# Performance work log

Measured on AMD Instinct MI355X. Metric: run time of the kernel, lower is better.

## Reference

```python
import jax, jax.numpy as jnp
import numpy as np

B = 4096
N_BUS = 118
N = B * N_BUS
E_ND = 4 * N
E = E_ND + N
REF_NODE = 0
NUM_GNN_LAYERS = 10


def setup_inputs() -> dict:
    key = jax.random.key(0)
    ks = jax.random.split(key, 8)
    x = jax.random.normal(ks[0], (N, 2), dtype=jnp.float32)
    y = jax.random.normal(ks[1], (N, 1), dtype=jnp.float32)
    edge_index_no_diag = jax.random.randint(ks[2], (2, E_ND), 0, N, dtype=jnp.int64)
    edge_attr_no_diag = jax.random.normal(ks[3], (E_ND,), dtype=jnp.float32)
    edge_index = jax.random.randint(ks[4], (2, E), 0, N, dtype=jnp.int64)
    edge_attr = jax.random.normal(ks[5], (E,), dtype=jnp.float32)
    ybus = jax.random.normal(ks[6], (B, N_BUS, N_BUS), dtype=jnp.float32)
    # ensure nonzero diagonal (bus self-admittance), as in real ybus matrices
    diag = 1.0 + jax.random.uniform(ks[7], (B, N_BUS), dtype=jnp.float32)
    ii = jnp.arange(N_BUS)
    ybus = ybus.at[:, ii, ii].set(diag)
    return {"x": x, "y": y, "edge_index_no_diag": edge_index_no_diag,
            "edge_attr_no_diag": edge_attr_no_diag, "edge_index": edge_index,
            "edge_attr": edge_attr, "ybus": ybus}


def _scatter_msg(theta, edge_index, edge_w):
    # message: y_j * edge_weight * 100, aggregated (add) at target node i
    src, dst = edge_index[0], edge_index[1]
    msg = theta[src, 0] * (edge_w * 100.0)
    return jax.ops.segment_sum(msg, dst, num_segments=N)[:, None]  # [N,1]


def reference(x, y, edge_index_no_diag, edge_attr_no_diag, edge_index, edge_attr, ybus):
    p = (x[:, 0] - x[:, 1])[:, None]                               # [N,1] net power injection
    denom = (jnp.diagonal(ybus, axis1=1, axis2=2) * 100.0).reshape(-1, 1)  # [N,1]

    def gpg_layer(theta):
        aggr = _scatter_msg(theta, edge_index_no_diag, edge_attr_no_diag)
        out = (p - aggr) / denom                                   # [N,1]
        o = out.reshape(B, N_BUS)
        o = o - o[:, REF_NODE:REF_NODE + 1]                        # subtract slack-bus angle
        return o.reshape(-1, 1)

    def lc_error(theta):
        aggr = _scatter_msg(theta, edge_index, edge_attr)
        return jnp.abs(p - aggr).sum()

    theta = jnp.zeros_like(y)
    out = gpg_layer(theta)
    errors = [lc_error(out)]
    for _ in range(NUM_GNN_LAYERS):
        out = gpg_layer(out)
        errors.append(lc_error(out))
    return out, jnp.stack(errors)
```

## Files before the change

kernel.cpp:

```cpp
#include <hip/hip_runtime.h>

#define NBUS 118
#define BATCH 4096
#define NN (BATCH * NBUS)
#define END_E (4 * NN)
#define EF_E (END_E + NN)
#define NLAYERS 10

#define NBKT 236
#define SPAN_SHIFT 11
#define SPAN_MASK 2047
#define TILE 4096
#define ND_TILES (END_E / TILE)
#define F_TILES  (EF_E / TILE)
#define CAP_ND 8960
#define CAP_F  11008

__global__ void init_kernel(const float* __restrict__ x,
                            const float* __restrict__ ybus,
                            float* __restrict__ p,
                            float* __restrict__ denomInv,
                            int* __restrict__ cursor_nd,
                            int* __restrict__ cursor_f,
                            float* __restrict__ errOut) {
    int tid = blockIdx.x * blockDim.x + threadIdx.x;
    int stride = gridDim.x * blockDim.x;
    for (int i = tid; i < NN; i += stride) {
        float2 xi = ((const float2*)x)[i];
        p[i] = xi.x - xi.y;
        int b = i / NBUS;
        int j = i - b * NBUS;
        denomInv[i] = 1.0f / (ybus[b * (NBUS * NBUS) + j * (NBUS + 1)] * 100.0f);
    }
    if (tid < 256) {
        cursor_nd[tid] = tid * CAP_ND;
        cursor_f[tid]  = tid * CAP_F;
    }
    if (tid < NLAYERS + 1) errOut[tid] = 0.0f;
}

__global__ __launch_bounds__(256) void binA_kernel(
        const int* __restrict__ src_nd, const int* __restrict__ dst_nd,
        const float* __restrict__ ea_nd,
        const int* __restrict__ src_f, const int* __restrict__ dst_f,
        const float* __restrict__ ea_f,
        int* __restrict__ cursor_nd, int* __restrict__ cursor_f,
        uint2* __restrict__ stg_nd, uint2* __restrict__ stg_f) {
    __shared__ uint2 buf[TILE];
    __shared__ unsigned char sb[TILE];
    __shared__ int hist[256];
    __shared__ int scanA[256];
    __shared__ int segStart[256];
    __shared__ int segGBase[256];

    bool isF = blockIdx.x >= ND_TILES;
    int tile = isF ? (blockIdx.x - ND_TILES) : blockIdx.x;
    const int* src = isF ? src_f : src_nd;
    const int* dst = isF ? dst_f : dst_nd;
    const float* ea = isF ? ea_f : ea_nd;
    int* cursor = isF ? cursor_f : cursor_nd;
    uint2* stg = isF ? stg_f : stg_nd;
    int cap = isF ? CAP_F : CAP_ND;

    int tid = threadIdx.x;
    int base = tile * TILE;

    hist[tid] = 0;
    __syncthreads();

    #pragma unroll
    for (int k = 0; k < TILE / 256; ++k) {
        int d = dst[base + k * 256 + tid];
        atomicAdd(&hist[d >> SPAN_SHIFT], 1);
    }
    __syncthreads();

    int cnt = hist[tid];
    scanA[tid] = cnt;
    __syncthreads();
    for (int off = 1; off < 256; off <<= 1) {
        int t = (tid >= off) ? scanA[tid - off] : 0;
        __syncthreads();
        scanA[tid] += t;
        __syncthreads();
    }
    int excl = scanA[tid] - cnt;
    segStart[tid] = excl;
    hist[tid] = excl;
    if (tid < NBKT && cnt > 0) segGBase[tid] = atomicAdd(&cursor[tid], cnt);
    __syncthreads();

    #pragma unroll
    for (int k = 0; k < TILE / 256; ++k) {
        int e = base + k * 256 + tid;
        int d = dst[e];
        int bkt = d >> SPAN_SHIFT;
        int pos = atomicAdd(&hist[bkt], 1);
        unsigned dl = (unsigned)(d & SPAN_MASK);
        buf[pos] = make_uint2((unsigned)src[e] | (dl << 19),
                              (unsigned)__float_as_int(ea[e] * 100.0f));
        sb[pos] = (unsigned char)bkt;
    }
    __syncthreads();

    #pragma unroll
    for (int k = 0; k < TILE / 256; ++k) {
        int slot = k * 256 + tid;
        int bkt = sb[slot];
        int gpos = segGBase[bkt] + (slot - segStart[bkt]);
        if (gpos < (bkt + 1) * cap)
            stg[gpos] = buf[slot];
    }
}

__global__ void bucket_base_kernel(const int* __restrict__ cursor_nd,
                                   const int* __restrict__ cursor_f,
                                   int* __restrict__ base_nd,
                                   int* __restrict__ base_f,
                                   int* __restrict__ start_nd,
                                   int* __restrict__ start_f) {
    __shared__ int sd[256];
    int tid = threadIdx.x;
    int c = 0;
    if (tid < NBKT) {
        c = cursor_nd[tid] - tid * CAP_ND;
        if (c > CAP_ND) c = CAP_ND;
    }
    sd[tid] = c;
    __syncthreads();
    for (int off = 1; off < 256; off <<= 1) {
        int t = (tid >= off) ? sd[tid - off] : 0;
        __syncthreads();
        sd[tid] += t;
        __syncthreads();
    }
    if (tid < NBKT) base_nd[tid] = sd[tid] - c;
    __syncthreads();
    if (tid < NBKT) {
        c = cursor_f[tid] - tid * CAP_F;
        if (c > CAP_F) c = CAP_F;
    } else c = 0;
    sd[tid] = c;
    __syncthreads();
    for (int off = 1; off < 256; off <<= 1) {
        int t = (tid >= off) ? sd[tid - off] : 0;
        __syncthreads();
        sd[tid] += t;
        __syncthreads();
    }
    if (tid < NBKT) base_f[tid] = sd[tid] - c;
    if (tid == 0) {
        start_nd[NN] = END_E;
        start_f[NN] = EF_E;
    }
}

__global__ __launch_bounds__(256) void binB_kernel(
        const uint2* __restrict__ stg_nd, const uint2* __restrict__ stg_f,
        const int* __restrict__ cursor_nd, const int* __restrict__ cursor_f,
        const int* __restrict__ base_nd, const int* __restrict__ base_f,
        int* __restrict__ start_nd, int* __restrict__ start_f,
        int2* __restrict__ perm_nd, int2* __restrict__ perm_f) {
    __shared__ int h[2048];
    __shared__ int partial[256];

    bool isF = blockIdx.x >= NBKT;
    int bb = isF ? (blockIdx.x - NBKT) : blockIdx.x;
    const uint2* stg = isF ? stg_f : stg_nd;
    int cap = isF ? CAP_F : CAP_ND;
    int cnt = (isF ? cursor_f[bb] : cursor_nd[bb]) - bb * cap;
    if (cnt > cap) cnt = cap;
    int denseBase = isF ? base_f[bb] : base_nd[bb];
    int* start = isF ? start_f : start_nd;
    int2* perm = isF ? perm_f : perm_nd;
    int stgBase = bb * cap;
    int tid = threadIdx.x;

    #pragma unroll
    for (int k = 0; k < 8; ++k) h[k * 256 + tid] = 0;
    __syncthreads();

    for (int i = tid; i < cnt; i += 256) {
        uint2 v = stg[stgBase + i];
        atomicAdd(&h[(v.x >> 19) & SPAN_MASK], 1);
    }
    __syncthreads();

    int loc[8];
    int s = 0;
    #pragma unroll
    for (int k = 0; k < 8; ++k) { loc[k] = h[tid * 8 + k]; s += loc[k]; }
    partial[tid] = s;
    __syncthreads();
    for (int off = 1; off < 256; off <<= 1) {
        int t = (tid >= off) ? partial[tid - off] : 0;
        __syncthreads();
        partial[tid] += t;
        __syncthreads();
    }
    int run = partial[tid] - s;
    #pragma unroll
    for (int k = 0; k < 8; ++k) { int c = loc[k]; h[tid * 8 + k] = run; run += c; }
    __syncthreads();

    int nodeBase = bb * 2048;
    #pragma unroll
    for (int k = 0; k < 8; ++k) {
        int l = k * 256 + tid;
        start[nodeBase + l] = denseBase + h[l];
    }
    __syncthreads();

    for (int i = tid; i < cnt; i += 256) {
        uint2 v = stg[stgBase + i];
        int dl = (v.x >> 19) & SPAN_MASK;
        int pos = denseBase + atomicAdd(&h[dl], 1);
        perm[pos] = make_int2((int)(v.x & 0x7FFFF), (int)v.y);
    }
}

__global__ void out0_kernel(const float* __restrict__ p,
                            const float* __restrict__ denomInv,
                            float* __restrict__ out) {
    int b = blockIdx.x;
    int j = threadIdx.x;
    int i = b * NBUS + j;
    __shared__ float z0;
    float z = 0.0f;
    if (j < NBUS) z = p[i] * denomInv[i];
    if (j == 0) z0 = z;
    __syncthreads();
    if (j < NBUS) out[i] = z - z0;
}

template <bool DO_OUT>
__global__ void layer_kernel(const int* __restrict__ start_nd,
                             const int2* __restrict__ perm_nd,
                             const int* __restrict__ start_f,
                             const int2* __restrict__ perm_f,
                             const float* __restrict__ cur,
                             const float* __restrict__ p,
                             const float* __restrict__ denomInv,
                             float* __restrict__ out,
                             float* __restrict__ errSlot) {
    int b = blockIdx.x;
    int j = threadIdx.x;
    int i = b * NBUS + j;
    bool act = j < NBUS;
    __shared__ float z0;
    __shared__ float ws2[2];

    float pv = 0.0f, di = 0.0f;
    float sum_nd = 0.0f, sum_f = 0.0f;
    if (act) {
        pv = p[i];
        if (DO_OUT) {
            di = denomInv[i];
            int s = start_nd[i], e = start_nd[i + 1];
            for (int t = s; t < e; ++t) {
                int2 pr = perm_nd[t];
                sum_nd += cur[pr.x] * __int_as_float(pr.y);
            }
        }
        int s = start_f[i], e = start_f[i + 1];
        for (int t = s; t < e; ++t) {
            int2 pr = perm_f[t];
            sum_f += cur[pr.x] * __int_as_float(pr.y);
        }
    }
    if (DO_OUT) {
        float z = (pv - sum_nd) * di;
        if (j == 0) z0 = z;
        __syncthreads();
        if (act) out[i] = z - z0;
    }
    float acc = act ? fabsf(pv - sum_f) : 0.0f;
    for (int off = 32; off > 0; off >>= 1) acc += __shfl_down(acc, off, 64);
    if ((threadIdx.x & 63) == 0) ws2[threadIdx.x >> 6] = acc;
    __syncthreads();
    if (threadIdx.x == 0) atomicAdd(errSlot, ws2[0] + ws2[1]);
}

extern "C" void kernel_launch(void* const* d_in, const int* in_sizes, int n_in,
                              void* d_out, int out_size, void* d_ws, size_t ws_size,
                              hipStream_t stream) {
    const float* x     = (const float*)d_in[0];
    const int*   ei_nd = (const int*)d_in[2];
    const float* ea_nd = (const float*)d_in[3];
    const int*   ei    = (const int*)d_in[4];
    const float* ea    = (const float*)d_in[5];
    const float* ybus  = (const float*)d_in[6];

    float* out_f = (float*)d_out;
    float* errs  = out_f + NN;

    float* wsf       = (float*)d_ws;
    float* p         = wsf;          wsf += NN;
    float* denomInv  = wsf;          wsf += NN;
    float* outA      = wsf;          wsf += NN;
    float* outB      = wsf;          wsf += NN;
    int*   start_nd  = (int*)wsf;    wsf += NN + 2;
    int*   start_f   = (int*)wsf;    wsf += NN + 2;
    int*   cursor_nd = (int*)wsf;    wsf += 256;
    int*   cursor_f  = (int*)wsf;    wsf += 256;
    int*   base_nd   = (int*)wsf;    wsf += 256;
    int*   base_f    = (int*)wsf;    wsf += 256;
    int2*  perm_nd   = (int2*)wsf;   wsf += 2LL * END_E;
    int2*  perm_f    = (int2*)wsf;   wsf += 2LL * EF_E;
    uint2* stg_nd    = (uint2*)wsf;  wsf += 2LL * NBKT * CAP_ND;
    uint2* stg_f     = (uint2*)wsf;  wsf += 2LL * NBKT * CAP_F;

    const int* src_nd = ei_nd;
    const int* dst_nd = ei_nd + END_E;
    const int* src_f  = ei;
    const int* dst_f  = ei + EF_E;

    init_kernel<<<1024, 256, 0, stream>>>(x, ybus, p, denomInv, cursor_nd, cursor_f, errs);
    binA_kernel<<<ND_TILES + F_TILES, 256, 0, stream>>>(
        src_nd, dst_nd, ea_nd, src_f, dst_f, ea,
        cursor_nd, cursor_f, stg_nd, stg_f);
    bucket_base_kernel<<<1, 256, 0, stream>>>(cursor_nd, cursor_f,
                                              base_nd, base_f, start_nd, start_f);
    binB_kernel<<<2 * NBKT, 256, 0, stream>>>(
        stg_nd, stg_f, cursor_nd, cursor_f, base_nd, base_f,
        start_nd, start_f, perm_nd, perm_f);

    out0_kernel<<<BATCH, 128, 0, stream>>>(p, denomInv, outA);
    const float* cur = outA;
    for (int k = 1; k <= NLAYERS; ++k) {
        float* nxt = (k == NLAYERS) ? out_f : ((k & 1) ? outB : outA);
        layer_kernel<true><<<BATCH, 128, 0, stream>>>(
            start_nd, perm_nd, start_f, perm_f, cur, p, denomInv, nxt, errs + (k - 1));
        cur = nxt;
    }
    layer_kernel<false><<<BATCH, 128, 0, stream>>>(
        start_nd, perm_nd, start_f, perm_f, cur, p, denomInv, nullptr, errs + NLAYERS);
}
```

Measured before the change: 1.332 ms.

## Replace CSR edge lists with padded ELL slots plus overflow tail

Switches the per-node edge storage from CSR (start offsets plus a dense permutation) to a column-major ELL layout with fixed width (8 for the non-diagonal graph, 9 for the full graph). Rows that need more slots spill into a tail array, reached through a flagged last slot. This removes the bucket-base scan kernel, and the layer kernels get coalesced, unrolled slot loads instead of variable-length loops. In exchange, init must zero a large ELL buffer and the padded slots read cur[0]*0. Tail capacity is fixed, so silent truncation is possible if it overflows.

Measured after the change: 1.299 ms. 1.02x faster.

```diff
diff --git a/kernel.cpp b/kernel.cpp
--- a/kernel.cpp
+++ b/kernel.cpp
@@ -16,13 +16,20 @@
 #define CAP_ND 8960
 #define CAP_F  11008
 
+#define W_ND 8
+#define W_F 9
+#define TAILCAP 1048576
+
 __global__ void init_kernel(const float* __restrict__ x,
                             const float* __restrict__ ybus,
                             float* __restrict__ p,
                             float* __restrict__ denomInv,
                             int* __restrict__ cursor_nd,
                             int* __restrict__ cursor_f,
+                            int* __restrict__ tailCur,
+                            int4* __restrict__ ellZero,
                             float* __restrict__ errOut) {
+    const int ZTOT4 = (2 * W_ND * NN + 2 * W_F * NN) / 4;
     int tid = blockIdx.x * blockDim.x + threadIdx.x;
     int stride = gridDim.x * blockDim.x;
     for (int i = tid; i < NN; i += stride) {
@@ -32,10 +39,12 @@
         int j = i - b * NBUS;
         denomInv[i] = 1.0f / (ybus[b * (NBUS * NBUS) + j * (NBUS + 1)] * 100.0f);
     }
+    for (int i = tid; i < ZTOT4; i += stride) ellZero[i] = make_int4(0, 0, 0, 0);
     if (tid < 256) {
         cursor_nd[tid] = tid * CAP_ND;
         cursor_f[tid]  = tid * CAP_F;
     }
+    if (tid < 2) tailCur[tid] = 0;
     if (tid < NLAYERS + 1) errOut[tid] = 0.0f;
 }
 
@@ -113,109 +122,67 @@
     }
 }
 
-__global__ void bucket_base_kernel(const int* __restrict__ cursor_nd,
-                                   const int* __restrict__ cursor_f,
-                                   int* __restrict__ base_nd,
-                                   int* __restrict__ base_f,
-                                   int* __restrict__ start_nd,
-                                   int* __restrict__ start_f) {
-    __shared__ int sd[256];
-    int tid = threadIdx.x;
-    int c = 0;
-    if (tid < NBKT) {
-        c = cursor_nd[tid] - tid * CAP_ND;
-        if (c > CAP_ND) c = CAP_ND;
-    }
-    sd[tid] = c;
-    __syncthreads();
-    for (int off = 1; off < 256; off <<= 1) {
-        int t = (tid >= off) ? sd[tid - off] : 0;
-        __syncthreads();
-        sd[tid] += t;
-        __syncthreads();
-    }
-    if (tid < NBKT) base_nd[tid] = sd[tid] - c;
-    __syncthreads();
-    if (tid < NBKT) {
-        c = cursor_f[tid] - tid * CAP_F;
-        if (c > CAP_F) c = CAP_F;
-    } else c = 0;
-    sd[tid] = c;
-    __syncthreads();
-    for (int off = 1; off < 256; off <<= 1) {
-        int t = (tid >= off) ? sd[tid - off] : 0;
-        __syncthreads();
-        sd[tid] += t;
-        __syncthreads();
-    }
-    if (tid < NBKT) base_f[tid] = sd[tid] - c;
-    if (tid == 0) {
-        start_nd[NN] = END_E;
-        start_f[NN] = EF_E;
-    }
-}
-
 __global__ __launch_bounds__(256) void binB_kernel(
         const uint2* __restrict__ stg_nd, const uint2* __restrict__ stg_f,
         const int* __restrict__ cursor_nd, const int* __restrict__ cursor_f,
-        const int* __restrict__ base_nd, const int* __restrict__ base_f,
-        int* __restrict__ start_nd, int* __restrict__ start_f,
-        int2* __restrict__ perm_nd, int2* __restrict__ perm_f) {
+        int2* __restrict__ ellND, int2* __restrict__ ellF,
+        int2* __restrict__ tailND, int2* __restrict__ tailF,
+        int* __restrict__ tailCur ) {
     __shared__ int h[2048];
-    __shared__ int partial[256];
+    __shared__ int rk[2048];
+    __shared__ int tb[2048];
 
     bool isF = blockIdx.x >= NBKT;
     int bb = isF ? (blockIdx.x - NBKT) : blockIdx.x;
     const uint2* stg = isF ? stg_f : stg_nd;
     int cap = isF ? CAP_F : CAP_ND;
-    int cnt = (isF ? cursor_f[bb] : cursor_nd[bb]) - bb * cap;
-    if (cnt > cap) cnt = cap;
-    int denseBase = isF ? base_f[bb] : base_nd[bb];
-    int* start = isF ? start_f : start_nd;
-    int2* perm = isF ? perm_f : perm_nd;
+    int W = isF ? W_F : W_ND;
+    int2* ell = isF ? ellF : ellND;
+    int2* tail = isF ? tailF : tailND;
+    int* tc = isF ? (tailCur + 1) : tailCur;
+    int cnt_all = (isF ? cursor_f[bb] : cursor_nd[bb]) - bb * cap;
+    if (cnt_all > cap) cnt_all = cap;
     int stgBase = bb * cap;
+    int nodeBase = bb * 2048;
     int tid = threadIdx.x;
 
     #pragma unroll
-    for (int k = 0; k < 8; ++k) h[k * 256 + tid] = 0;
-    __syncthreads();
-
-    for (int i = tid; i < cnt; i += 256) {
+    for (int k = 0; k < 8; ++k) { h[k * 256 + tid] = 0; rk[k * 256 + tid] = 0; }
+    __syncthreads();
+
+    for (int i = tid; i < cnt_all; i += 256) {
         uint2 v = stg[stgBase + i];
         atomicAdd(&h[(v.x >> 19) & SPAN_MASK], 1);
     }
     __syncthreads();
 
-    int loc[8];
-    int s = 0;
-    #pragma unroll
-    for (int k = 0; k < 8; ++k) { loc[k] = h[tid * 8 + k]; s += loc[k]; }
-    partial[tid] = s;
-    __syncthreads();
-    for (int off = 1; off < 256; off <<= 1) {
-        int t = (tid >= off) ? partial[tid - off] : 0;
-        __syncthreads();
-        partial[tid] += t;
-        __syncthreads();
-    }
-    int run = partial[tid] - s;
-    #pragma unroll
-    for (int k = 0; k < 8; ++k) { int c = loc[k]; h[tid * 8 + k] = run; run += c; }
-    __syncthreads();
-
-    int nodeBase = bb * 2048;
     #pragma unroll
     for (int k = 0; k < 8; ++k) {
-        int l = k * 256 + tid;
-        start[nodeBase + l] = denseBase + h[l];
-    }
-    __syncthreads();
-
-    for (int i = tid; i < cnt; i += 256) {
+        int dl = k * 256 + tid;
+        int c = h[dl];
+        if (c > W) {
+            int len = c - (W - 1);
+            int tbase = atomicAdd(tc, len);
+            if (tbase + len > TAILCAP) { tbase = 0; len = 0; }
+            tb[dl] = tbase;
+            ell[(W - 1) * NN + nodeBase + dl] =
+                make_int2((int)(0x80000000u | (unsigned)len), tbase);
+        }
+    }
+    __syncthreads();
+
+    for (int i = tid; i < cnt_all; i += 256) {
         uint2 v = stg[stgBase + i];
         int dl = (v.x >> 19) & SPAN_MASK;
-        int pos = denseBase + atomicAdd(&h[dl], 1);
-        perm[pos] = make_int2((int)(v.x & 0x7FFFF), (int)v.y);
+        int c = h[dl];
+        int r = atomicAdd(&rk[dl], 1);
+        int plain = (c <= W) ? c : (W - 1);
+        int2 pr = make_int2((int)(v.x & 0x7FFFF), (int)v.y);
+        if (r < plain) ell[r * NN + nodeBase + dl] = pr;
+        else {
+            int pos = tb[dl] + r - plain;
+            if (pos < TAILCAP) tail[pos] = pr;
+        }
     }
 }
 
@@ -234,15 +201,14 @@
 }
 
 template <bool DO_OUT>
-__global__ void layer_kernel(const int* __restrict__ start_nd,
-                             const int2* __restrict__ perm_nd,
-                             const int* __restrict__ start_f,
-                             const int2* __restrict__ perm_f,
-                             const float* __restrict__ cur,
-                             const float* __restrict__ p,
-                             const float* __restrict__ denomInv,
-                             float* __restrict__ out,
-                             float* __restrict__ errSlot) {
+__global__ __launch_bounds__(128) void layer_kernel(
+        const int2* __restrict__ ellND, const int2* __restrict__ tailND,
+        const int2* __restrict__ ellF, const int2* __restrict__ tailF,
+        const float* __restrict__ cur,
+        const float* __restrict__ p,
+        const float* __restrict__ denomInv,
+        float* __restrict__ out,
+        float* __restrict__ errSlot) {
     int b = blockIdx.x;
     int j = threadIdx.x;
     int i = b * NBUS + j;
@@ -256,16 +222,42 @@
         pv = p[i];
         if (DO_OUT) {
             di = denomInv[i];
-            int s = start_nd[i], e = start_nd[i + 1];
-            for (int t = s; t < e; ++t) {
-                int2 pr = perm_nd[t];
-                sum_nd += cur[pr.x] * __int_as_float(pr.y);
+            int2 e[W_ND];
+            #pragma unroll
+            for (int s = 0; s < W_ND - 1; ++s) e[s] = ellND[s * NN + i];
+            #pragma unroll
+            for (int s = 0; s < W_ND - 1; ++s)
+                sum_nd += cur[e[s].x] * __int_as_float(e[s].y);
+            int2 last = ellND[(W_ND - 1) * NN + i];
+            if (last.x < 0) {
+                int len = last.x & 0x7FFFFFFF;
+                int tbase = last.y;
+                for (int t = 0; t < len; ++t) {
+                    int2 pr = tailND[tbase + t];
+                    sum_nd += cur[pr.x] * __int_as_float(pr.y);
+                }
+            } else {
+                sum_nd += cur[last.x] * __int_as_float(last.y);
             }
         }
-        int s = start_f[i], e = start_f[i + 1];
-        for (int t = s; t < e; ++t) {
-            int2 pr = perm_f[t];
-            sum_f += cur[pr.x] * __int_as_float(pr.y);
+        {
+            int2 e[W_F];
+            #pragma unroll
+            for (int s = 0; s < W_F - 1; ++s) e[s] = ellF[s * NN + i];
+            #pragma unroll
+            for (int s = 0; s < W_F - 1; ++s)
+                sum_f += cur[e[s].x] * __int_as_float(e[s].y);
+            int2 last = ellF[(W_F - 1) * NN + i];
+            if (last.x < 0) {
+                int len = last.x & 0x7FFFFFFF;
+                int tbase = last.y;
+                for (int t = 0; t < len; ++t) {
+                    int2 pr = tailF[tbase + t];
+                    sum_f += cur[pr.x] * __int_as_float(pr.y);
+                }
+            } else {
+                sum_f += cur[last.x] * __int_as_float(last.y);
+            }
         }
     }
     if (DO_OUT) {
@@ -299,14 +291,13 @@
     float* denomInv  = wsf;          wsf += NN;
     float* outA      = wsf;          wsf += NN;
     float* outB      = wsf;          wsf += NN;
-    int*   start_nd  = (int*)wsf;    wsf += NN + 2;
-    int*   start_f   = (int*)wsf;    wsf += NN + 2;
     int*   cursor_nd = (int*)wsf;    wsf += 256;
     int*   cursor_f  = (int*)wsf;    wsf += 256;
-    int*   base_nd   = (int*)wsf;    wsf += 256;
-    int*   base_f    = (int*)wsf;    wsf += 256;
-    int2*  perm_nd   = (int2*)wsf;   wsf += 2LL * END_E;
-    int2*  perm_f    = (int2*)wsf;   wsf += 2LL * EF_E;
+    int*   tailCur   = (int*)wsf;    wsf += 4;
+    int2*  ellND     = (int2*)wsf;   wsf += 2LL * W_ND * NN;
+    int2*  ellF      = (int2*)wsf;   wsf += 2LL * W_F * NN;
+    int2*  tailND    = (int2*)wsf;   wsf += 2LL * TAILCAP;
+    int2*  tailF     = (int2*)wsf;   wsf += 2LL * TAILCAP;
     uint2* stg_nd    = (uint2*)wsf;  wsf += 2LL * NBKT * CAP_ND;
     uint2* stg_f     = (uint2*)wsf;  wsf += 2LL * NBKT * CAP_F;
 
@@ -315,24 +306,24 @@
     const int* src_f  = ei;
     const int* dst_f  = ei + EF_E;
 
-    init_kernel<<<1024, 256, 0, stream>>>(x, ybus, p, denomInv, cursor_nd, cursor_f, errs);
+    init_kernel<<<2048, 256, 0, stream>>>(x, ybus, p, denomInv,
+                                          cursor_nd, cursor_f, tailCur,
+                                          (int4*)ellND, errs);
     binA_kernel<<<ND_TILES + F_TILES, 256, 0, stream>>>(
         src_nd, dst_nd, ea_nd, src_f, dst_f, ea,
         cursor_nd, cursor_f, stg_nd, stg_f);
-    bucket_base_kernel<<<1, 256, 0, stream>>>(cursor_nd, cursor_f,
-                                              base_nd, base_f, start_nd, start_f);
     binB_kernel<<<2 * NBKT, 256, 0, stream>>>(
-        stg_nd, stg_f, cursor_nd, cursor_f, base_nd, base_f,
-        start_nd, start_f, perm_nd, perm_f);
+        stg_nd, stg_f, cursor_nd, cursor_f,
+        ellND, ellF, tailND, tailF, tailCur);
 
     out0_kernel<<<BATCH, 128, 0, stream>>>(p, denomInv, outA);
     const float* cur = outA;
     for (int k = 1; k <= NLAYERS; ++k) {
         float* nxt = (k == NLAYERS) ? out_f : ((k & 1) ? outB : outA);
         layer_kernel<true><<<BATCH, 128, 0, stream>>>(
-            start_nd, perm_nd, start_f, perm_f, cur, p, denomInv, nxt, errs + (k - 1));
+            ellND, tailND, ellF, tailF, cur, p, denomInv, nxt, errs + (k - 1));
         cur = nxt;
     }
     layer_kernel<false><<<BATCH, 128, 0, stream>>>(
-        start_nd, perm_nd, start_f, perm_f, cur, p, denomInv, nullptr, errs + NLAYERS);
-}
+        ellND, tailND, ellF, tailF, cur, p, denomInv, nullptr, errs + NLAYERS);
+}
```
